# Optimization experiments

Hardware: AMD Instinct MI355X
Metric: run time of the kernel (lower is better)

Reference implementation:

```python
import jax, jax.numpy as jnp
import numpy as np

B, NR, NG = 16, 96, 64
AF, BF = 98, 6
H, QM, MAXNB, DEPTH = 300, 160, 10, 4
P = 2048
F = 2 * H + QM          # 760
D0 = F + 10             # 770


def _graph_idx(k, batch, n, idx_max):
    # gather_nd style indices (batch_idx, neighbor_idx): [batch, n, MAXNB, 2]
    nbr = jax.random.randint(k, (batch, n, MAXNB), 0, idx_max)
    b = jnp.broadcast_to(jnp.arange(batch)[:, None, None], (batch, n, MAXNB))
    return jnp.stack([b, nbr], axis=-1)


def setup_inputs() -> dict:
    key = jax.random.key(0)
    ks = jax.random.split(key, 32)
    f32 = jnp.float32
    inp = {}
    inp['res_atom'] = jax.random.normal(ks[0], (B, NR, AF), f32)
    inp['res_bond'] = jax.random.normal(ks[1], (B, NR, BF), f32)
    inp['res_atom_graph'] = _graph_idx(ks[2], B, NR, NR)
    inp['res_bond_graph'] = _graph_idx(ks[3], B, NR, NR)
    inp['res_num_nbs'] = jax.random.randint(ks[4], (B, NR), 1, MAXNB + 1)
    inp['res_node_mask'] = jnp.ones((B, NR, 1), f32)
    inp['rg_atom'] = jax.random.normal(ks[5], (B, NG, AF), f32)
    inp['rg_bond'] = jax.random.normal(ks[6], (B, NG, BF), f32)
    inp['rg_atom_graph'] = _graph_idx(ks[7], B, NG, NG)
    inp['rg_bond_graph'] = _graph_idx(ks[8], B, NG, NG)
    inp['rg_num_nbs'] = jax.random.randint(ks[9], (B, NG), 1, MAXNB + 1)
    inp['rg_node_mask'] = jnp.ones((B, NG, 1), f32)
    seg = jnp.repeat(jnp.arange(B), P // B)  # sorted reaction ids for segment_mean
    i = jax.random.randint(ks[10], (P,), 0, NR)
    j = jax.random.randint(ks[11], (P,), 0, NR)
    inp['core_mask'] = jnp.stack([seg, i, j], axis=-1)[None]   # [1, P, 3]
    inp['fatom_qm'] = jax.random.normal(ks[12], (B, NR, QM), f32)
    inp['connect'] = jax.random.normal(ks[13], (1, P, 10), f32)
    STD = 0.1  # keep relu chains alive at depth 4
    w = lambda k, shape: STD * jax.random.normal(k, shape, f32)
    for pre, kk in (('res', 14), ('rg', 20)):
        inp[pre + '_W_atom'] = w(ks[kk], (AF, H))
        inp[pre + '_W_nei_atom'] = w(ks[kk + 1], (H, H))
        inp[pre + '_W_nei_bond'] = w(ks[kk + 2], (BF, H))
        inp[pre + '_W_self'] = w(ks[kk + 3], (H, H))
        inp[pre + '_W_U2'] = w(ks[kk + 4], (H + BF, H))
        inp[pre + '_W_U1'] = w(ks[kk + 5], (2 * H, H))
    inp['W_att_h'] = w(ks[26], (H, H))
    inp['W_att_s'] = w(ks[27], (H, 1))
    inp['W_score0'] = 0.01 * jax.random.normal(ks[28], (D0, D0), f32)
    inp['W_score'] = 0.01 * jax.random.normal(ks[29], (D0, 1), f32)
    return inp


def _wln(atom, bond, atom_graph, bond_graph, num_nbs, node_mask,
         W_atom, W_nei_atom, W_nei_bond, W_self, W_U2, W_U1):
    relu = jax.nn.relu
    af = relu(atom @ W_atom)                                       # [B,N,H]
    mask = (jnp.arange(MAXNB)[None, None, :] < num_nbs[:, :, None])
    mask = mask.astype(af.dtype)[..., None]                        # [B,N,MAXNB,1]
    for _ in range(DEPTH):
        fa = af[atom_graph[..., 0], atom_graph[..., 1]]            # [B,N,MAXNB,H]
        fb = bond[bond_graph[..., 0], bond_graph[..., 1]]          # [B,N,MAXNB,BF]
        h_nei = relu(fa @ W_nei_atom) * relu(fb @ W_nei_bond)
        f_nei = jnp.sum(h_nei * mask, axis=2)                      # masked nbr sum
        kernels = f_nei * relu(af @ W_self) * node_mask
        pre = relu(jnp.concatenate([fa, fb], axis=3) @ W_U2)
        nei_label = jnp.sum(pre * mask, axis=2)
        af = relu(jnp.concatenate([af, nei_label], axis=2) @ W_U1)
    return kernels


def _forward(res_atom, res_bond, res_atom_graph, res_bond_graph, res_num_nbs, res_node_mask,
             rg_atom, rg_bond, rg_atom_graph, rg_bond_graph, rg_num_nbs, rg_node_mask,
             core_mask, fatom_qm, connect,
             res_W_atom, res_W_nei_atom, res_W_nei_bond, res_W_self, res_W_U2, res_W_U1,
             rg_W_atom, rg_W_nei_atom, rg_W_nei_bond, rg_W_self, rg_W_U2, rg_W_U1,
             W_att_h, W_att_s, W_score0, W_score):
    res_h = _wln(res_atom, res_bond, res_atom_graph, res_bond_graph, res_num_nbs, res_node_mask,
                 res_W_atom, res_W_nei_atom, res_W_nei_bond, res_W_self, res_W_U2, res_W_U1)
    rg_h = _wln(rg_atom, rg_bond, rg_atom_graph, rg_bond_graph, rg_num_nbs, rg_node_mask,
                rg_W_atom, rg_W_nei_atom, rg_W_nei_bond, rg_W_self, rg_W_U2, rg_W_U1)
    # Global attention: broadcast pairwise sum reactant x reagent atoms
    pair_att = res_h[:, :, None, :] + rg_h[:, None, :, :]          # [B,NR,NG,H]
    att = jax.nn.sigmoid(jax.nn.relu(pair_att @ W_att_h) @ W_att_s)
    ctx = jnp.sum(att * rg_h[:, None, :, :], axis=2)               # [B,NR,H]
    h = jnp.concatenate([res_h, ctx, fatom_qm], axis=-1)           # [B,NR,F]
    cm = core_mask[0]                                              # [P,3] = (b,i,j)
    # atom_pair[b,i,j] = h[b,i] + h[b,j]; gather only the core pairs (no N^2 tensor)
    pair = h[cm[:, 0], cm[:, 1]] + h[cm[:, 0], cm[:, 2]]           # [P,F]
    rh = jax.nn.relu(jnp.concatenate([pair, connect[0]], axis=-1) @ W_score0)
    seg = cm[:, 0]
    sums = jax.ops.segment_sum(rh, seg, num_segments=B)
    cnt = jax.ops.segment_sum(jnp.ones((P,), rh.dtype), seg, num_segments=B)
    mean = sums / cnt[:, None]                                     # segment_mean
    return mean @ W_score                                          # [B,1]


def reference(res_atom, res_bond, res_atom_graph, res_bond_graph, res_num_nbs, res_node_mask,
              rg_atom, rg_bond, rg_atom_graph, rg_bond_graph, rg_num_nbs, rg_node_mask,
              core_mask, fatom_qm, connect,
              res_W_atom, res_W_nei_atom, res_W_nei_bond, res_W_self, res_W_U2, res_W_U1,
              rg_W_atom, rg_W_nei_atom, rg_W_nei_bond, rg_W_self, rg_W_U2, rg_W_U1,
              W_att_h, W_att_s, W_score0, W_score):
    return _forward(res_atom, res_bond, res_atom_graph, res_bond_graph, res_num_nbs, res_node_mask,
                    rg_atom, rg_bond, rg_atom_graph, rg_bond_graph, rg_num_nbs, rg_node_mask,
                    core_mask, fatom_qm, connect,
                    res_W_atom, res_W_nei_atom, res_W_nei_bond, res_W_self, res_W_U2, res_W_U1,
                    rg_W_atom, rg_W_nei_atom, rg_W_nei_bond, rg_W_self, rg_W_U2, rg_W_U1,
                    W_att_h, W_att_s, W_score0, W_score)
```

## Files before the change

kernel.cpp:

```cpp
#include <hip/hip_runtime.h>


constexpr int cB = 16, cNR = 96, cNG = 64;
constexpr int cAF = 98, cBF = 6;
constexpr int cH = 300, cQM = 160, cMAXNB = 10, cDEPTH = 4;
constexpr int cP = 2048;
constexpr int cF = 2 * cH + cQM;
constexpr int cD0 = cF + 10;

constexpr int Mres = cB * cNR;
constexpr int Mrg  = cB * cNG;

typedef __attribute__((ext_vector_type(8))) short v8s;
typedef __attribute__((ext_vector_type(4))) float v4f;

__device__ inline unsigned short f2bf(float f) {
  unsigned u = __float_as_uint(f);
  u += 0x7FFF + ((u >> 16) & 1);
  return (unsigned short)(u >> 16);
}
__device__ inline float bf2f(unsigned short s) {
  return __uint_as_float(((unsigned)s) << 16);
}

struct PrepArg { const float* W; unsigned short* hiT; unsigned short* loT; int K; int N; int Kpad; };
struct PrepArgs { PrepArg a[16]; };

__global__ __launch_bounds__(256) void prep_k(PrepArgs pa)
{
  PrepArg p = pa.a[blockIdx.z];
  int idx = blockIdx.x * 256 + threadIdx.x;
  int total = p.N * p.Kpad;
  if (idx >= total) return;
  int n = idx / p.Kpad, k = idx - n * p.Kpad;
  float w = (k < p.K) ? p.W[(size_t)k * p.N + n] : 0.f;
  unsigned short h = f2bf(w);
  p.hiT[idx] = h;
  p.loT[idx] = f2bf(w - bf2f(h));
}

struct GArg {
  const float* A; const float* A2;
  const unsigned short* W1h; const unsigned short* W1l;
  const unsigned short* W2h; const unsigned short* W2l;
  float* C; int M; int K1; int Kp1; int K2; int Kp2; int act;
};
struct GArgs6 { GArg a[6]; };

#define MFMA __builtin_amdgcn_mfma_f32_16x16x32_bf16

__global__ __launch_bounds__(256) void gemm_mfma(GArgs6 ga, int N)
{
  GArg g = ga.a[blockIdx.z];
  int m0 = blockIdx.y * 64;
  if (m0 >= g.M) return;
  int n0 = blockIdx.x * 64;
  int nT = (g.Kp1 + g.Kp2) >> 5;

  __shared__ unsigned short Ah[2][64][40];
  __shared__ unsigned short Al[2][64][40];
  __shared__ unsigned short Bh[2][64][40];
  __shared__ unsigned short Bl[2][64][40];

  int tid = threadIdx.x;
  int sm = tid >> 2;
  int sk = (tid & 3) << 3;

  float areg[8];
  uint4 bh_reg, bl_reg;

  auto fetch = [&](int kv0) {
    int kv = kv0 + sk;
    const float* src; int kk, Klim;
    if (kv < g.Kp1) { src = g.A  + (size_t)(m0 + sm) * g.K1; kk = kv;          Klim = g.K1; }
    else            { src = g.A2 + (size_t)(m0 + sm) * g.K2; kk = kv - g.Kp1;  Klim = g.K2; }
    if (((Klim & 3) == 0) && kk + 7 < Klim) {
      float4 v0 = *(const float4*)(src + kk);
      float4 v1 = *(const float4*)(src + kk + 4);
      areg[0]=v0.x; areg[1]=v0.y; areg[2]=v0.z; areg[3]=v0.w;
      areg[4]=v1.x; areg[5]=v1.y; areg[6]=v1.z; areg[7]=v1.w;
    } else {
#pragma unroll
      for (int j = 0; j < 8; ++j) {
        int k = kk + j;
        areg[j] = (k < Klim) ? src[k] : 0.f;
      }
    }
    int gn = n0 + sm;
    if (gn < N) {
      const unsigned short *ph, *pl;
      if (kv < g.Kp1) { size_t o = (size_t)gn * g.Kp1 + kv;            ph = g.W1h + o; pl = g.W1l + o; }
      else            { size_t o = (size_t)gn * g.Kp2 + (kv - g.Kp1);  ph = g.W2h + o; pl = g.W2l + o; }
      bh_reg = *(const uint4*)ph;
      bl_reg = *(const uint4*)pl;
    } else {
      bh_reg = make_uint4(0,0,0,0); bl_reg = make_uint4(0,0,0,0);
    }
  };

  auto store = [&](int buf) {
    unsigned hs[8], ls[8];
#pragma unroll
    for (int j = 0; j < 8; ++j) {
      unsigned short h = f2bf(areg[j]);
      hs[j] = h;
      ls[j] = f2bf(areg[j] - bf2f(h));
    }
    uint4 hh, ll;
    hh.x = hs[0] | (hs[1] << 16); hh.y = hs[2] | (hs[3] << 16);
    hh.z = hs[4] | (hs[5] << 16); hh.w = hs[6] | (hs[7] << 16);
    ll.x = ls[0] | (ls[1] << 16); ll.y = ls[2] | (ls[3] << 16);
    ll.z = ls[4] | (ls[5] << 16); ll.w = ls[6] | (ls[7] << 16);
    *(uint4*)&Ah[buf][sm][sk] = hh;
    *(uint4*)&Al[buf][sm][sk] = ll;
    *(uint4*)&Bh[buf][sm][sk] = bh_reg;
    *(uint4*)&Bl[buf][sm][sk] = bl_reg;
  };

  int l = tid & 63, w = tid >> 6;
  int wm = (w >> 1) << 5, wn = (w & 1) << 5;
  int ar = wm + (l & 15), br = wn + (l & 15);
  int kc = (l >> 4) << 3;

  v4f acc00 = {0,0,0,0}, acc01 = {0,0,0,0}, acc10 = {0,0,0,0}, acc11 = {0,0,0,0};

  fetch(0); store(0); __syncthreads();
  for (int t = 0; t < nT; ++t) {
    if (t + 1 < nT) fetch((t + 1) << 5);
    int cur = t & 1;
    v8s ah0 = *(const v8s*)&Ah[cur][ar][kc];
    v8s ah1 = *(const v8s*)&Ah[cur][ar + 16][kc];
    v8s al0 = *(const v8s*)&Al[cur][ar][kc];
    v8s al1 = *(const v8s*)&Al[cur][ar + 16][kc];
    v8s bh0 = *(const v8s*)&Bh[cur][br][kc];
    v8s bh1 = *(const v8s*)&Bh[cur][br + 16][kc];
    v8s bl0 = *(const v8s*)&Bl[cur][br][kc];
    v8s bl1 = *(const v8s*)&Bl[cur][br + 16][kc];
    acc00 = MFMA(ah0, bh0, acc00, 0, 0, 0);
    acc00 = MFMA(ah0, bl0, acc00, 0, 0, 0);
    acc00 = MFMA(al0, bh0, acc00, 0, 0, 0);
    acc01 = MFMA(ah0, bh1, acc01, 0, 0, 0);
    acc01 = MFMA(ah0, bl1, acc01, 0, 0, 0);
    acc01 = MFMA(al0, bh1, acc01, 0, 0, 0);
    acc10 = MFMA(ah1, bh0, acc10, 0, 0, 0);
    acc10 = MFMA(ah1, bl0, acc10, 0, 0, 0);
    acc10 = MFMA(al1, bh0, acc10, 0, 0, 0);
    acc11 = MFMA(ah1, bh1, acc11, 0, 0, 0);
    acc11 = MFMA(ah1, bl1, acc11, 0, 0, 0);
    acc11 = MFMA(al1, bh1, acc11, 0, 0, 0);
    if (t + 1 < nT) store(cur ^ 1);
    __syncthreads();
  }

  int rbase = m0 + wm + ((l >> 4) << 2);
  int cbase = n0 + wn + (l & 15);
  auto wr = [&](v4f a, int fi, int fj) {
    int gn = cbase + fj * 16;
    if (gn >= N) return;
    float* Cp = g.C + (size_t)(rbase + fi * 16) * N + gn;
#pragma unroll
    for (int r = 0; r < 4; ++r) {
      float v = a[r];
      if (g.act) v = fmaxf(v, 0.f);
      Cp[(size_t)r * N] = v;
    }
  };
  wr(acc00, 0, 0); wr(acc01, 0, 1); wr(acc10, 1, 0); wr(acc11, 1, 1);
}

__global__ __launch_bounds__(256) void score_mfma_k(
    const float* __restrict__ h, const float* __restrict__ conn,
    const int* __restrict__ cm,
    const unsigned short* __restrict__ W0h, const unsigned short* __restrict__ W0l,
    const float* __restrict__ Wsc, float* __restrict__ pairsum)
{
  const int Kp = 800;
  const int nT = Kp >> 5;
  int m0 = blockIdx.y * 64;
  int n0 = blockIdx.x * 64;

  __shared__ unsigned short Ah[2][64][40];
  __shared__ unsigned short Al[2][64][40];
  __shared__ unsigned short Bh[2][64][40];
  __shared__ unsigned short Bl[2][64][40];

  int tid = threadIdx.x;
  int sm = tid >> 2;
  int sk = (tid & 3) << 3;

  int p = m0 + sm;
  int s3 = cm[p * 3 + 0];
  const float* h1 = h + (size_t)(s3 * cNR + cm[p * 3 + 1]) * cF;
  const float* h2 = h + (size_t)(s3 * cNR + cm[p * 3 + 2]) * cF;
  const float* cp = conn + (size_t)p * 10;

  float areg[8];
  uint4 bh_reg, bl_reg;

  auto fetch = [&](int kv0) {
    int kv = kv0 + sk;
    if (kv + 7 < cF) {
      float4 u = *(const float4*)(h1 + kv);
      float4 v = *(const float4*)(h2 + kv);
      float4 u2 = *(const float4*)(h1 + kv + 4);
      float4 v2 = *(const float4*)(h2 + kv + 4);
      areg[0]=u.x+v.x; areg[1]=u.y+v.y; areg[2]=u.z+v.z; areg[3]=u.w+v.w;
      areg[4]=u2.x+v2.x; areg[5]=u2.y+v2.y; areg[6]=u2.z+v2.z; areg[7]=u2.w+v2.w;
    } else {
#pragma unroll
      for (int j = 0; j < 8; ++j) {
        int k = kv + j;
        float v = 0.f;
        if (k < cF) v = h1[k] + h2[k];
        else if (k < cD0) v = cp[k - cF];
        areg[j] = v;
      }
    }
    int gn = n0 + sm;
    if (gn < cD0) {
      size_t o = (size_t)gn * Kp + kv;
      bh_reg = *(const uint4*)(W0h + o);
      bl_reg = *(const uint4*)(W0l + o);
    } else {
      bh_reg = make_uint4(0,0,0,0); bl_reg = make_uint4(0,0,0,0);
    }
  };

  auto store = [&](int buf) {
    unsigned hs[8], ls[8];
#pragma unroll
    for (int j = 0; j < 8; ++j) {
      unsigned short hv = f2bf(areg[j]);
      hs[j] = hv;
      ls[j] = f2bf(areg[j] - bf2f(hv));
    }
    uint4 hh, ll;
    hh.x = hs[0] | (hs[1] << 16); hh.y = hs[2] | (hs[3] << 16);
    hh.z = hs[4] | (hs[5] << 16); hh.w = hs[6] | (hs[7] << 16);
    ll.x = ls[0] | (ls[1] << 16); ll.y = ls[2] | (ls[3] << 16);
    ll.z = ls[4] | (ls[5] << 16); ll.w = ls[6] | (ls[7] << 16);
    *(uint4*)&Ah[buf][sm][sk] = hh;
    *(uint4*)&Al[buf][sm][sk] = ll;
    *(uint4*)&Bh[buf][sm][sk] = bh_reg;
    *(uint4*)&Bl[buf][sm][sk] = bl_reg;
  };

  int l = tid & 63, w = tid >> 6;
  int wm = (w >> 1) << 5, wn = (w & 1) << 5;
  int ar = wm + (l & 15), br = wn + (l & 15);
  int kc = (l >> 4) << 3;

  v4f acc00 = {0,0,0,0}, acc01 = {0,0,0,0}, acc10 = {0,0,0,0}, acc11 = {0,0,0,0};

  fetch(0); store(0); __syncthreads();
  for (int t = 0; t < nT; ++t) {
    if (t + 1 < nT) fetch((t + 1) << 5);
    int cur = t & 1;
    v8s ah0 = *(const v8s*)&Ah[cur][ar][kc];
    v8s ah1 = *(const v8s*)&Ah[cur][ar + 16][kc];
    v8s al0 = *(const v8s*)&Al[cur][ar][kc];
    v8s al1 = *(const v8s*)&Al[cur][ar + 16][kc];
    v8s bh0 = *(const v8s*)&Bh[cur][br][kc];
    v8s bh1 = *(const v8s*)&Bh[cur][br + 16][kc];
    v8s bl0 = *(const v8s*)&Bl[cur][br][kc];
    v8s bl1 = *(const v8s*)&Bl[cur][br + 16][kc];
    acc00 = MFMA(ah0, bh0, acc00, 0, 0, 0);
    acc00 = MFMA(ah0, bl0, acc00, 0, 0, 0);
    acc00 = MFMA(al0, bh0, acc00, 0, 0, 0);
    acc01 = MFMA(ah0, bh1, acc01, 0, 0, 0);
    acc01 = MFMA(ah0, bl1, acc01, 0, 0, 0);
    acc01 = MFMA(al0, bh1, acc01, 0, 0, 0);
    acc10 = MFMA(ah1, bh0, acc10, 0, 0, 0);
    acc10 = MFMA(ah1, bl0, acc10, 0, 0, 0);
    acc10 = MFMA(al1, bh0, acc10, 0, 0, 0);
    acc11 = MFMA(ah1, bh1, acc11, 0, 0, 0);
    acc11 = MFMA(ah1, bl1, acc11, 0, 0, 0);
    acc11 = MFMA(al1, bh1, acc11, 0, 0, 0);
    if (t + 1 < nT) store(cur ^ 1);
    __syncthreads();
  }

  int cbase = n0 + wn + (l & 15);
  float w0 = (cbase      < cD0) ? Wsc[cbase]      : 0.f;
  float w1 = (cbase + 16 < cD0) ? Wsc[cbase + 16] : 0.f;
  float ps[8];
#pragma unroll
  for (int r = 0; r < 4; ++r) {
    ps[r]     = fmaxf(acc00[r], 0.f) * w0 + fmaxf(acc01[r], 0.f) * w1;
    ps[4 + r] = fmaxf(acc10[r], 0.f) * w0 + fmaxf(acc11[r], 0.f) * w1;
  }
#pragma unroll
  for (int m = 1; m < 16; m <<= 1) {
#pragma unroll
    for (int q = 0; q < 8; ++q) ps[q] += __shfl_xor(ps[q], m, 64);
  }
  if ((l & 15) == 0) {
#pragma unroll
    for (int q = 0; q < 8; ++q) {
      int gm = m0 + wm + (q >> 2) * 16 + ((l >> 4) << 2) + (q & 3);
      atomicAdd(&pairsum[gm], ps[q]);
    }
  }
}

__global__ __launch_bounds__(320) void nei_label2_k(
    const float* __restrict__ RaR, const float* __restrict__ RbR,
    const int* __restrict__ agR, const int* __restrict__ bgR,
    const int* __restrict__ nnbR, float* __restrict__ outR,
    const float* __restrict__ RaG, const float* __restrict__ RbG,
    const int* __restrict__ agG, const int* __restrict__ bgG,
    const int* __restrict__ nnbG, float* __restrict__ outG)
{
  int node = blockIdx.x;
  const float *Ra, *Rb; const int *ag, *bg, *nnb; float* out; int Nn, loc;
  if (node < Mres) { Ra=RaR; Rb=RbR; ag=agR; bg=bgR; nnb=nnbR; out=outR; Nn=cNR; loc=node; }
  else { Ra=RaG; Rb=RbG; ag=agG; bg=bgG; nnb=nnbG; out=outG; Nn=cNG; loc=node-Mres; }
  int h = threadIdx.x;
  int nn = nnb[loc];
  const int* agp = ag + (size_t)loc * cMAXNB * 2;
  const int* bgp = bg + (size_t)loc * cMAXNB * 2;
  if (h < cH) {
    float s = 0.f;
    for (int k = 0; k < nn; ++k) {
      int ra = agp[2 * k] * Nn + agp[2 * k + 1];
      int rb = bgp[2 * k] * Nn + bgp[2 * k + 1];
      s += fmaxf(Ra[(size_t)ra * cH + h] + Rb[(size_t)rb * cH + h], 0.f);
    }
    out[(size_t)loc * cH + h] = s;
  }
}

__global__ __launch_bounds__(320) void kernels2_k(
    const float* __restrict__ SaR, const float* __restrict__ SbR,
    const float* __restrict__ SelfR_R,
    const int* __restrict__ agR, const int* __restrict__ bgR,
    const int* __restrict__ nnbR, const float* __restrict__ maskR,
    float* __restrict__ outR,
    const float* __restrict__ SaG, const float* __restrict__ SbG,
    const float* __restrict__ SelfR_G,
    const int* __restrict__ agG, const int* __restrict__ bgG,
    const int* __restrict__ nnbG, const float* __restrict__ maskG,
    float* __restrict__ outG)
{
  int node = blockIdx.x;
  const float *Sa, *Sb, *Se, *mk; const int *ag, *bg, *nnb; float* out; int Nn, loc;
  if (node < Mres) { Sa=SaR; Sb=SbR; Se=SelfR_R; ag=agR; bg=bgR; nnb=nnbR; mk=maskR; out=outR; Nn=cNR; loc=node; }
  else { Sa=SaG; Sb=SbG; Se=SelfR_G; ag=agG; bg=bgG; nnb=nnbG; mk=maskG; out=outG; Nn=cNG; loc=node-Mres; }
  int h = threadIdx.x;
  int nn = nnb[loc];
  const int* agp = ag + (size_t)loc * cMAXNB * 2;
  const int* bgp = bg + (size_t)loc * cMAXNB * 2;
  if (h < cH) {
    float s = 0.f;
    for (int k = 0; k < nn; ++k) {
      int ra = agp[2 * k] * Nn + agp[2 * k + 1];
      int rb = bgp[2 * k] * Nn + bgp[2 * k + 1];
      s += Sa[(size_t)ra * cH + h] * Sb[(size_t)rb * cH + h];
    }
    out[(size_t)loc * cH + h] = s * Se[(size_t)loc * cH + h] * mk[loc];
  }
}

#define AIT 4
__global__ __launch_bounds__(256) void att_ctx_h_k(
    const float* __restrict__ U, const float* __restrict__ V,
    const float* __restrict__ att_w, const float* __restrict__ rgh,
    const float* __restrict__ kern, const float* __restrict__ qm,
    float* __restrict__ h)
{
  __shared__ float attL[AIT][cNG];
  int blk = blockIdx.x;
  int b = blk / (cNR / AIT);
  int it = blk - b * (cNR / AIT);
  int row0 = b * cNR + it * AIT;
  int tid = threadIdx.x, lane = tid & 63, w = tid >> 6;
  int n0 = lane * 4, n1 = 256 + lane * 4;
  bool v1 = (lane < 11);
  float4 z4 = make_float4(0.f, 0.f, 0.f, 0.f);

  float4 u[AIT][2], wv[2];
  wv[0] = *(const float4*)(att_w + n0);
  wv[1] = v1 ? *(const float4*)(att_w + n1) : z4;
#pragma unroll
  for (int i = 0; i < AIT; ++i) {
    const float* Ur = U + (size_t)(row0 + i) * cH;
    u[i][0] = *(const float4*)(Ur + n0);
    u[i][1] = v1 ? *(const float4*)(Ur + n1) : z4;
  }

  for (int r = 0; r < 4; ++r) {
    int jb = w * 16 + r * 4;
    float4 vv[4][2];
#pragma unroll
    for (int q = 0; q < 4; ++q) {
      const float* Vr = V + (size_t)(b * cNG + jb + q) * cH;
      vv[q][0] = *(const float4*)(Vr + n0);
      vv[q][1] = v1 ? *(const float4*)(Vr + n1) : z4;
    }
    float s[4][AIT];
#pragma unroll
    for (int q = 0; q < 4; ++q)
#pragma unroll
      for (int i = 0; i < AIT; ++i) {
        float acc = 0.f;
#pragma unroll
        for (int pp = 0; pp < 2; ++pp) {
          float4 uu = u[i][pp], vq = vv[q][pp], ww = wv[pp];
          acc += fmaxf(uu.x + vq.x, 0.f) * ww.x;
          acc += fmaxf(uu.y + vq.y, 0.f) * ww.y;
          acc += fmaxf(uu.z + vq.z, 0.f) * ww.z;
          acc += fmaxf(uu.w + vq.w, 0.f) * ww.w;
        }
        s[q][i] = acc;
      }
#pragma unroll
    for (int m = 1; m < 64; m <<= 1)
#pragma unroll
      for (int q = 0; q < 4; ++q)
#pragma unroll
        for (int i = 0; i < AIT; ++i)
          s[q][i] += __shfl_xor(s[q][i], m);
    if (lane < 16) {
      float sv = 0.f;
#pragma unroll
      for (int q = 0; q < 4; ++q)
#pragma unroll
        for (int i = 0; i < AIT; ++i)
          if (lane == q * 4 + i) sv = s[q][i];
      attL[lane & 3][jb + (lane >> 2)] = 1.f / (1.f + expf(-sv));
    }
  }
  __syncthreads();

  const float* rgb = rgh + (size_t)b * cNG * cH;
  float* hrow = h + (size_t)(row0 + w) * cF;
  for (int c = lane; c < 75; c += 64) {
    float4 p = z4;
    for (int j = 0; j < cNG; ++j) {
      float aj = attL[w][j];
      float4 rv = *(const float4*)(rgb + (size_t)j * cH + c * 4);
      p.x += aj * rv.x; p.y += aj * rv.y; p.z += aj * rv.z; p.w += aj * rv.w;
    }
    *(float4*)(hrow + cH + c * 4) = p;
  }
  for (int idx = tid; idx < AIT * 75; idx += 256) {
    int i = idx / 75, c = idx - i * 75;
    *(float4*)(h + (size_t)(row0 + i) * cF + c * 4) =
        *(const float4*)(kern + (size_t)(row0 + i) * cH + c * 4);
  }
  for (int idx = tid; idx < AIT * 40; idx += 256) {
    int i = idx / 40, c = idx - i * 40;
    *(float4*)(h + (size_t)(row0 + i) * cF + 2 * cH + c * 4) =
        *(const float4*)(qm + (size_t)(row0 + i) * cQM + c * 4);
  }
}

__global__ void seg_final_k(const float* __restrict__ ps,
                            const int* __restrict__ cm, float* __restrict__ out)
{
  __shared__ float s[cB];
  int tid = threadIdx.x;
  if (tid < cB) s[tid] = 0.f;
  __syncthreads();
  for (int p = tid; p < cP; p += 256) atomicAdd(&s[cm[p * 3]], ps[p]);
  __syncthreads();
  if (tid < cB) out[tid] = s[tid] * (1.f / 128.f);
}

extern "C" void kernel_launch(void* const* d_in, const int* in_sizes, int n_in,
                              void* d_out, int out_size, void* d_ws, size_t ws_size,
                              hipStream_t stream)
{
  (void)in_sizes; (void)n_in; (void)out_size; (void)ws_size;
  const float* res_atom = (const float*)d_in[0];
  const float* res_bond = (const float*)d_in[1];
  const int*   res_ag   = (const int*)d_in[2];
  const int*   res_bg   = (const int*)d_in[3];
  const int*   res_nnb  = (const int*)d_in[4];
  const float* res_mask = (const float*)d_in[5];
  const float* rg_atom  = (const float*)d_in[6];
  const float* rg_bond  = (const float*)d_in[7];
  const int*   rg_ag    = (const int*)d_in[8];
  const int*   rg_bg    = (const int*)d_in[9];
  const int*   rg_nnb   = (const int*)d_in[10];
  const float* rg_mask  = (const float*)d_in[11];
  const int*   core     = (const int*)d_in[12];
  const float* qm       = (const float*)d_in[13];
  const float* connect  = (const float*)d_in[14];
  const float* Wm[2][6];
  for (int s = 0; s < 2; ++s)
    for (int k = 0; k < 6; ++k) Wm[s][k] = (const float*)d_in[15 + s * 6 + k];
  const float* W_att_h  = (const float*)d_in[27];
  const float* W_att_s  = (const float*)d_in[28];
  const float* W_score0 = (const float*)d_in[29];
  const float* W_score  = (const float*)d_in[30];
  float* out = (float*)d_out;

  float* ws = (float*)d_ws;
  size_t off = 0;
  auto alloc = [&](size_t nfloat) {
    float* p = ws + off;
    off += (nfloat + 63) & ~(size_t)63;
    return p;
  };
  auto allocU = [&](size_t nush) {
    return (unsigned short*)alloc((nush + 1) / 2);
  };

  float* afA_r = alloc((size_t)Mres * cH);
  float* afB_r = alloc((size_t)Mres * cH);
  float* Rb_r  = alloc((size_t)Mres * cH);
  float* Sb_r  = alloc((size_t)Mres * cH);
  float* Ra_r  = alloc((size_t)Mres * cH);
  float* nei_r = alloc((size_t)Mres * cH);
  float* kern_r= alloc((size_t)Mres * cH);
  float* afA_g = alloc((size_t)Mrg * cH);
  float* afB_g = alloc((size_t)Mrg * cH);
  float* Rb_g  = alloc((size_t)Mrg * cH);
  float* Sb_g  = alloc((size_t)Mrg * cH);
  float* Ra_g  = alloc((size_t)Mrg * cH);
  float* nei_g = alloc((size_t)Mrg * cH);
  float* kern_g= alloc((size_t)Mrg * cH);
  float* U     = alloc((size_t)Mres * cH);
  float* V     = alloc((size_t)Mrg * cH);
  float* h760  = alloc((size_t)Mres * cF);
  float* pairsum = alloc(cP);

  struct WT { unsigned short *h, *l; int K, Kp; const float* src; };
  auto rup32 = [](int k) { return (k + 31) & ~31; };
  WT t[2][8];
  for (int s = 0; s < 2; ++s) {
    const int Ks[8] = {cAF, cH, cBF, cH, cH, cBF, cH, cH};
    const float* srcs[8] = {
      Wm[s][0], Wm[s][1], Wm[s][2], Wm[s][3],
      Wm[s][4], Wm[s][4] + (size_t)cH * cH,
      Wm[s][5], Wm[s][5] + (size_t)cH * cH };
    for (int k = 0; k < 8; ++k) {
      int Kp = rup32(Ks[k]);
      t[s][k].K = Ks[k]; t[s][k].Kp = Kp; t[s][k].src = srcs[k];
      t[s][k].h = allocU((size_t)cH * Kp);
      t[s][k].l = allocU((size_t)cH * Kp);
    }
  }
  unsigned short* attT_h = allocU((size_t)cH * 320);
  unsigned short* attT_l = allocU((size_t)cH * 320);
  unsigned short* sc0T_h = allocU((size_t)cD0 * 800);
  unsigned short* sc0T_l = allocU((size_t)cD0 * 800);

  {
    PrepArgs pa{};
    for (int s = 0; s < 2; ++s)
      for (int k = 0; k < 8; ++k)
        pa.a[s * 8 + k] = {t[s][k].src, t[s][k].h, t[s][k].l, t[s][k].K, cH, t[s][k].Kp};
    dim3 grid((cH * 320 + 255) / 256, 1, 16);
    prep_k<<<grid, dim3(256), 0, stream>>>(pa);
  }
  {
    PrepArgs pa{};
    pa.a[0] = {W_att_h,  attT_h, attT_l, cH, cH, 320};
    pa.a[1] = {W_score0, sc0T_h, sc0T_l, cD0, cD0, 800};
    dim3 grid((cD0 * 800 + 255) / 256, 1, 2);
    prep_k<<<grid, dim3(256), 0, stream>>>(pa);
  }

  dim3 blk(256);
  GArg zero{};
  auto launch = [&](GArgs6& ga, int nprob) {
    dim3 grid(5, Mres / 64, nprob);
    gemm_mfma<<<grid, blk, 0, stream>>>(ga, cH);
  };

  {
    GArgs6 ga{{
      {res_atom, nullptr, t[0][0].h, t[0][0].l, nullptr, nullptr, afA_r, Mres, cAF, 128, 0, 0, 1},
      {rg_atom,  nullptr, t[1][0].h, t[1][0].l, nullptr, nullptr, afA_g, Mrg,  cAF, 128, 0, 0, 1},
      {res_bond, nullptr, t[0][5].h, t[0][5].l, nullptr, nullptr, Rb_r,  Mres, cBF, 32,  0, 0, 0},
      {rg_bond,  nullptr, t[1][5].h, t[1][5].l, nullptr, nullptr, Rb_g,  Mrg,  cBF, 32,  0, 0, 0},
      {res_bond, nullptr, t[0][2].h, t[0][2].l, nullptr, nullptr, Sb_r,  Mres, cBF, 32,  0, 0, 1},
      {rg_bond,  nullptr, t[1][2].h, t[1][2].l, nullptr, nullptr, Sb_g,  Mrg,  cBF, 32,  0, 0, 1},
    }};
    launch(ga, 6);
  }

  float* af_r = afA_r; float* afo_r = afB_r;
  float* af_g = afA_g; float* afo_g = afB_g;
  for (int it = 0; it < cDEPTH - 1; ++it) {
    {
      GArgs6 ga{{
        {af_r, nullptr, t[0][4].h, t[0][4].l, nullptr, nullptr, Ra_r, Mres, cH, 320, 0, 0, 0},
        {af_g, nullptr, t[1][4].h, t[1][4].l, nullptr, nullptr, Ra_g, Mrg,  cH, 320, 0, 0, 0},
        zero, zero, zero, zero,
      }};
      launch(ga, 2);
    }
    nei_label2_k<<<dim3(Mres + Mrg), dim3(320), 0, stream>>>(
        Ra_r, Rb_r, res_ag, res_bg, res_nnb, nei_r,
        Ra_g, Rb_g, rg_ag, rg_bg, rg_nnb, nei_g);
    {
      GArgs6 ga{{
        {af_r, nei_r, t[0][6].h, t[0][6].l, t[0][7].h, t[0][7].l, afo_r, Mres, cH, 320, cH, 320, 1},
        {af_g, nei_g, t[1][6].h, t[1][6].l, t[1][7].h, t[1][7].l, afo_g, Mrg,  cH, 320, cH, 320, 1},
        zero, zero, zero, zero,
      }};
      launch(ga, 2);
    }
    { float* tmp = af_r; af_r = afo_r; afo_r = tmp; }
    { float* tmp = af_g; af_g = afo_g; afo_g = tmp; }
  }

  {
    GArgs6 ga{{
      {af_r, nullptr, t[0][1].h, t[0][1].l, nullptr, nullptr, Ra_r,  Mres, cH, 320, 0, 0, 1},
      {af_g, nullptr, t[1][1].h, t[1][1].l, nullptr, nullptr, Ra_g,  Mrg,  cH, 320, 0, 0, 1},
      {af_r, nullptr, t[0][3].h, t[0][3].l, nullptr, nullptr, nei_r, Mres, cH, 320, 0, 0, 1},
      {af_g, nullptr, t[1][3].h, t[1][3].l, nullptr, nullptr, nei_g, Mrg,  cH, 320, 0, 0, 1},
      zero, zero,
    }};
    launch(ga, 4);
  }
  kernels2_k<<<dim3(Mres + Mrg), dim3(320), 0, stream>>>(
      Ra_r, Sb_r, nei_r, res_ag, res_bg, res_nnb, res_mask, kern_r,
      Ra_g, Sb_g, nei_g, rg_ag, rg_bg, rg_nnb, rg_mask, kern_g);

  {
    GArgs6 ga{{
      {kern_r, nullptr, attT_h, attT_l, nullptr, nullptr, U, Mres, cH, 320, 0, 0, 0},
      {kern_g, nullptr, attT_h, attT_l, nullptr, nullptr, V, Mrg,  cH, 320, 0, 0, 0},
      zero, zero, zero, zero,
    }};
    launch(ga, 2);
  }
  att_ctx_h_k<<<dim3(cB * (cNR / AIT)), dim3(256), 0, stream>>>(
      U, V, W_att_s, kern_g, kern_r, qm, h760);

  hipMemsetAsync(pairsum, 0, cP * sizeof(float), stream);
  score_mfma_k<<<dim3(13, cP / 64), blk, 0, stream>>>(
      h760, connect, core, sc0T_h, sc0T_l, W_score, pairsum);
  seg_final_k<<<dim3(1), dim3(256), 0, stream>>>(pairsum, core, out);
}
```

Measured before the change: 270.3 us.

## Fuse neighbor gather into GEMM A-load and concatenate weight matrices

Removes the separate neighbor-label kernel: the U1 GEMM now builds its A operand on the fly by gathering and summing relu(Ra+Rb) over neighbors. The self half of U1 is computed in the same GEMM as W_U2 through concatenated weights, and its result is added as a bias in the epilogue. Final-stage Ra/self GEMMs are likewise merged into one N=600 GEMM. The two prep launches and the pairsum memset are folded into a single prep kernel. The cost is redundant gather work: every N-column block of the GEMM recomputes the same neighbor sums.

```diff
diff --git a/kernel.cpp b/kernel.cpp
--- a/kernel.cpp
+++ b/kernel.cpp
@@ -23,27 +23,34 @@
   return __uint_as_float(((unsigned)s) << 16);
 }
 
-struct PrepArg { const float* W; unsigned short* hiT; unsigned short* loT; int K; int N; int Kpad; };
-struct PrepArgs { PrepArg a[16]; };
+struct PrepEnt { const float* W; unsigned short* hiT; unsigned short* loT;
+                 int K, N, Kpad; };
+struct PrepArgs { PrepEnt e[19]; int bases[20]; int nent; };
 
 __global__ __launch_bounds__(256) void prep_k(PrepArgs pa)
 {
-  PrepArg p = pa.a[blockIdx.z];
-  int idx = blockIdx.x * 256 + threadIdx.x;
-  int total = p.N * p.Kpad;
-  if (idx >= total) return;
-  int n = idx / p.Kpad, k = idx - n * p.Kpad;
+  int g = blockIdx.x * 256 + threadIdx.x;
+  if (g >= pa.bases[pa.nent]) return;
+  int idx = 0;
+  while (g >= pa.bases[idx + 1]) ++idx;
+  PrepEnt p = pa.e[idx];
+  int local = g - pa.bases[idx];
+  if (!p.W) { ((float*)p.hiT)[local] = 0.f; return; }
+  int n = local / p.Kpad, k = local - n * p.Kpad;
   float w = (k < p.K) ? p.W[(size_t)k * p.N + n] : 0.f;
   unsigned short h = f2bf(w);
-  p.hiT[idx] = h;
-  p.loT[idx] = f2bf(w - bf2f(h));
+  p.hiT[local] = h;
+  p.loT[local] = f2bf(w - bf2f(h));
 }
 
 struct GArg {
-  const float* A; const float* A2;
-  const unsigned short* W1h; const unsigned short* W1l;
-  const unsigned short* W2h; const unsigned short* W2l;
-  float* C; int M; int K1; int Kp1; int K2; int Kp2; int act;
+  const float* A;
+  const float* Ra; const float* Rb;
+  const int* ag; const int* bg; const int* nnb; int NnIdx; int ldRa;
+  const unsigned short* Wh; const unsigned short* Wl;
+  const float* bias; int ldBias;
+  float* C; int ldC;
+  int M, K, Kp, act;
 };
 struct GArgs6 { GArg a[6]; };
 
@@ -55,7 +62,7 @@
   int m0 = blockIdx.y * 64;
   if (m0 >= g.M) return;
   int n0 = blockIdx.x * 64;
-  int nT = (g.Kp1 + g.Kp2) >> 5;
+  int nT = g.Kp >> 5;
 
   __shared__ unsigned short Ah[2][64][40];
   __shared__ unsigned short Al[2][64][40];
@@ -65,34 +72,63 @@
   int tid = threadIdx.x;
   int sm = tid >> 2;
   int sk = (tid & 3) << 3;
+  int gm = m0 + sm;
+
+  int nn = 0; const int *agp = nullptr, *bgp = nullptr;
+  if (!g.A) {
+    nn = g.nnb[gm];
+    agp = g.ag + (size_t)gm * 2 * cMAXNB;
+    bgp = g.bg + (size_t)gm * 2 * cMAXNB;
+  }
 
   float areg[8];
   uint4 bh_reg, bl_reg;
 
   auto fetch = [&](int kv0) {
-    int kv = kv0 + sk;
-    const float* src; int kk, Klim;
-    if (kv < g.Kp1) { src = g.A  + (size_t)(m0 + sm) * g.K1; kk = kv;          Klim = g.K1; }
-    else            { src = g.A2 + (size_t)(m0 + sm) * g.K2; kk = kv - g.Kp1;  Klim = g.K2; }
-    if (((Klim & 3) == 0) && kk + 7 < Klim) {
-      float4 v0 = *(const float4*)(src + kk);
-      float4 v1 = *(const float4*)(src + kk + 4);
-      areg[0]=v0.x; areg[1]=v0.y; areg[2]=v0.z; areg[3]=v0.w;
-      areg[4]=v1.x; areg[5]=v1.y; areg[6]=v1.z; areg[7]=v1.w;
+    int kk = kv0 + sk;
+    if (g.A) {
+      const float* src = g.A + (size_t)gm * g.K;
+      if (((g.K & 3) == 0) && kk + 7 < g.K) {
+        float4 v0 = *(const float4*)(src + kk);
+        float4 v1 = *(const float4*)(src + kk + 4);
+        areg[0]=v0.x; areg[1]=v0.y; areg[2]=v0.z; areg[3]=v0.w;
+        areg[4]=v1.x; areg[5]=v1.y; areg[6]=v1.z; areg[7]=v1.w;
+      } else {
+#pragma unroll
+        for (int j = 0; j < 8; ++j) areg[j] = (kk + j < g.K) ? src[kk + j] : 0.f;
+      }
     } else {
-#pragma unroll
-      for (int j = 0; j < 8; ++j) {
-        int k = kk + j;
-        areg[j] = (k < Klim) ? src[k] : 0.f;
+      float acc[8] = {0.f,0.f,0.f,0.f,0.f,0.f,0.f,0.f};
+      if (kk < g.K) {
+        for (int k = 0; k < nn; ++k) {
+          int ra = agp[2 * k] * g.NnIdx + agp[2 * k + 1];
+          int rb = bgp[2 * k] * g.NnIdx + bgp[2 * k + 1];
+          const float* pa = g.Ra + (size_t)ra * g.ldRa + kk;
+          const float* pb = g.Rb + (size_t)rb * cH + kk;
+          float4 a0 = *(const float4*)pa, a1 = *(const float4*)(pa + 4);
+          float4 b0 = *(const float4*)pb, b1 = *(const float4*)(pb + 4);
+          acc[0] += fmaxf(a0.x + b0.x, 0.f);
+          acc[1] += fmaxf(a0.y + b0.y, 0.f);
+          acc[2] += fmaxf(a0.z + b0.z, 0.f);
+          acc[3] += fmaxf(a0.w + b0.w, 0.f);
+          acc[4] += fmaxf(a1.x + b1.x, 0.f);
+          acc[5] += fmaxf(a1.y + b1.y, 0.f);
+          acc[6] += fmaxf(a1.z + b1.z, 0.f);
+          acc[7] += fmaxf(a1.w + b1.w, 0.f);
+        }
+        if (kk + 8 > g.K) {
+#pragma unroll
+          for (int j = 0; j < 8; ++j) if (kk + j >= g.K) acc[j] = 0.f;
+        }
       }
+#pragma unroll
+      for (int j = 0; j < 8; ++j) areg[j] = acc[j];
     }
     int gn = n0 + sm;
     if (gn < N) {
-      const unsigned short *ph, *pl;
-      if (kv < g.Kp1) { size_t o = (size_t)gn * g.Kp1 + kv;            ph = g.W1h + o; pl = g.W1l + o; }
-      else            { size_t o = (size_t)gn * g.Kp2 + (kv - g.Kp1);  ph = g.W2h + o; pl = g.W2l + o; }
-      bh_reg = *(const uint4*)ph;
-      bl_reg = *(const uint4*)pl;
+      size_t o = (size_t)gn * g.Kp + kv0 + sk;
+      bh_reg = *(const uint4*)(g.Wh + o);
+      bl_reg = *(const uint4*)(g.Wl + o);
     } else {
       bh_reg = make_uint4(0,0,0,0); bl_reg = make_uint4(0,0,0,0);
     }
@@ -102,9 +138,9 @@
     unsigned hs[8], ls[8];
 #pragma unroll
     for (int j = 0; j < 8; ++j) {
-      unsigned short h = f2bf(areg[j]);
-      hs[j] = h;
-      ls[j] = f2bf(areg[j] - bf2f(h));
+      unsigned short hv = f2bf(areg[j]);
+      hs[j] = hv;
+      ls[j] = f2bf(areg[j] - bf2f(hv));
     }
     uint4 hh, ll;
     hh.x = hs[0] | (hs[1] << 16); hh.y = hs[2] | (hs[3] << 16);
@@ -157,12 +193,15 @@
   auto wr = [&](v4f a, int fi, int fj) {
     int gn = cbase + fj * 16;
     if (gn >= N) return;
-    float* Cp = g.C + (size_t)(rbase + fi * 16) * N + gn;
+    float* Cp = g.C + (size_t)(rbase + fi * 16) * g.ldC + gn;
+    const float* Bp = g.bias ? g.bias + (size_t)(rbase + fi * 16) * g.ldBias + gn
+                             : nullptr;
 #pragma unroll
     for (int r = 0; r < 4; ++r) {
       float v = a[r];
+      if (Bp) v += Bp[(size_t)r * g.ldBias];
       if (g.act) v = fmaxf(v, 0.f);
-      Cp[(size_t)r * N] = v;
+      Cp[(size_t)r * g.ldC] = v;
     }
   };
   wr(acc00, 0, 0); wr(acc01, 0, 1); wr(acc10, 1, 0); wr(acc11, 1, 1);
@@ -303,18 +342,20 @@
   }
 }
 
-__global__ __launch_bounds__(320) void nei_label2_k(
-    const float* __restrict__ RaR, const float* __restrict__ RbR,
+__global__ __launch_bounds__(320) void kernels2_k(
+    const float* __restrict__ SaSeR, const float* __restrict__ SbR,
     const int* __restrict__ agR, const int* __restrict__ bgR,
-    const int* __restrict__ nnbR, float* __restrict__ outR,
-    const float* __restrict__ RaG, const float* __restrict__ RbG,
+    const int* __restrict__ nnbR, const float* __restrict__ maskR,
+    float* __restrict__ outR,
+    const float* __restrict__ SaSeG, const float* __restrict__ SbG,
     const int* __restrict__ agG, const int* __restrict__ bgG,
-    const int* __restrict__ nnbG, float* __restrict__ outG)
+    const int* __restrict__ nnbG, const float* __restrict__ maskG,
+    float* __restrict__ outG)
 {
   int node = blockIdx.x;
-  const float *Ra, *Rb; const int *ag, *bg, *nnb; float* out; int Nn, loc;
-  if (node < Mres) { Ra=RaR; Rb=RbR; ag=agR; bg=bgR; nnb=nnbR; out=outR; Nn=cNR; loc=node; }
-  else { Ra=RaG; Rb=RbG; ag=agG; bg=bgG; nnb=nnbG; out=outG; Nn=cNG; loc=node-Mres; }
+  const float *SaSe, *Sb, *mk; const int *ag, *bg, *nnb; float* out; int Nn, loc;
+  if (node < Mres) { SaSe=SaSeR; Sb=SbR; ag=agR; bg=bgR; nnb=nnbR; mk=maskR; out=outR; Nn=cNR; loc=node; }
+  else { SaSe=SaSeG; Sb=SbG; ag=agG; bg=bgG; nnb=nnbG; mk=maskG; out=outG; Nn=cNG; loc=node-Mres; }
   int h = threadIdx.x;
   int nn = nnb[loc];
   const int* agp = ag + (size_t)loc * cMAXNB * 2;
@@ -324,40 +365,9 @@
     for (int k = 0; k < nn; ++k) {
       int ra = agp[2 * k] * Nn + agp[2 * k + 1];
       int rb = bgp[2 * k] * Nn + bgp[2 * k + 1];
-      s += fmaxf(Ra[(size_t)ra * cH + h] + Rb[(size_t)rb * cH + h], 0.f);
-    }
-    out[(size_t)loc * cH + h] = s;
-  }
-}
-
-__global__ __launch_bounds__(320) void kernels2_k(
-    const float* __restrict__ SaR, const float* __restrict__ SbR,
-    const float* __restrict__ SelfR_R,
-    const int* __restrict__ agR, const int* __restrict__ bgR,
-    const int* __restrict__ nnbR, const float* __restrict__ maskR,
-    float* __restrict__ outR,
-    const float* __restrict__ SaG, const float* __restrict__ SbG,
-    const float* __restrict__ SelfR_G,
-    const int* __restrict__ agG, const int* __restrict__ bgG,
-    const int* __restrict__ nnbG, const float* __restrict__ maskG,
-    float* __restrict__ outG)
-{
-  int node = blockIdx.x;
-  const float *Sa, *Sb, *Se, *mk; const int *ag, *bg, *nnb; float* out; int Nn, loc;
-  if (node < Mres) { Sa=SaR; Sb=SbR; Se=SelfR_R; ag=agR; bg=bgR; nnb=nnbR; mk=maskR; out=outR; Nn=cNR; loc=node; }
-  else { Sa=SaG; Sb=SbG; Se=SelfR_G; ag=agG; bg=bgG; nnb=nnbG; mk=maskG; out=outG; Nn=cNG; loc=node-Mres; }
-  int h = threadIdx.x;
-  int nn = nnb[loc];
-  const int* agp = ag + (size_t)loc * cMAXNB * 2;
-  const int* bgp = bg + (size_t)loc * cMAXNB * 2;
-  if (h < cH) {
-    float s = 0.f;
-    for (int k = 0; k < nn; ++k) {
-      int ra = agp[2 * k] * Nn + agp[2 * k + 1];
-      int rb = bgp[2 * k] * Nn + bgp[2 * k + 1];
-      s += Sa[(size_t)ra * cH + h] * Sb[(size_t)rb * cH + h];
-    }
-    out[(size_t)loc * cH + h] = s * Se[(size_t)loc * cH + h] * mk[loc];
+      s += SaSe[(size_t)ra * 600 + h] * Sb[(size_t)rb * cH + h];
+    }
+    out[(size_t)loc * cH + h] = s * SaSe[(size_t)loc * 600 + 300 + h] * mk[loc];
   }
 }
 
@@ -507,79 +517,100 @@
     return (unsigned short*)alloc((nush + 1) / 2);
   };
 
-  float* afA_r = alloc((size_t)Mres * cH);
-  float* afB_r = alloc((size_t)Mres * cH);
-  float* Rb_r  = alloc((size_t)Mres * cH);
-  float* Sb_r  = alloc((size_t)Mres * cH);
-  float* Ra_r  = alloc((size_t)Mres * cH);
-  float* nei_r = alloc((size_t)Mres * cH);
-  float* kern_r= alloc((size_t)Mres * cH);
-  float* afA_g = alloc((size_t)Mrg * cH);
-  float* afB_g = alloc((size_t)Mrg * cH);
-  float* Rb_g  = alloc((size_t)Mrg * cH);
-  float* Sb_g  = alloc((size_t)Mrg * cH);
-  float* Ra_g  = alloc((size_t)Mrg * cH);
-  float* nei_g = alloc((size_t)Mrg * cH);
-  float* kern_g= alloc((size_t)Mrg * cH);
-  float* U     = alloc((size_t)Mres * cH);
-  float* V     = alloc((size_t)Mrg * cH);
-  float* h760  = alloc((size_t)Mres * cF);
+  float* afA_r  = alloc((size_t)Mres * cH);
+  float* afB_r  = alloc((size_t)Mres * cH);
+  float* Rb_r   = alloc((size_t)Mres * cH);
+  float* Sb_r   = alloc((size_t)Mres * cH);
+  float* RaU1_r = alloc((size_t)Mres * 600);
+  float* kern_r = alloc((size_t)Mres * cH);
+  float* afA_g  = alloc((size_t)Mrg * cH);
+  float* afB_g  = alloc((size_t)Mrg * cH);
+  float* Rb_g   = alloc((size_t)Mrg * cH);
+  float* Sb_g   = alloc((size_t)Mrg * cH);
+  float* RaU1_g = alloc((size_t)Mrg * 600);
+  float* kern_g = alloc((size_t)Mrg * cH);
+  float* U      = alloc((size_t)Mres * cH);
+  float* V      = alloc((size_t)Mrg * cH);
+  float* h760   = alloc((size_t)Mres * cF);
   float* pairsum = alloc(cP);
 
-  struct WT { unsigned short *h, *l; int K, Kp; const float* src; };
-  auto rup32 = [](int k) { return (k + 31) & ~31; };
-  WT t[2][8];
+  unsigned short *atomT_h[2], *atomT_l[2], *nbT_h[2], *nbT_l[2];
+  unsigned short *U2bT_h[2], *U2bT_l[2], *cat1_h[2], *cat1_l[2];
+  unsigned short *cat2_h[2], *cat2_l[2], *U1bT_h[2], *U1bT_l[2];
   for (int s = 0; s < 2; ++s) {
-    const int Ks[8] = {cAF, cH, cBF, cH, cH, cBF, cH, cH};
-    const float* srcs[8] = {
-      Wm[s][0], Wm[s][1], Wm[s][2], Wm[s][3],
-      Wm[s][4], Wm[s][4] + (size_t)cH * cH,
-      Wm[s][5], Wm[s][5] + (size_t)cH * cH };
-    for (int k = 0; k < 8; ++k) {
-      int Kp = rup32(Ks[k]);
-      t[s][k].K = Ks[k]; t[s][k].Kp = Kp; t[s][k].src = srcs[k];
-      t[s][k].h = allocU((size_t)cH * Kp);
-      t[s][k].l = allocU((size_t)cH * Kp);
-    }
-  }
-  unsigned short* attT_h = allocU((size_t)cH * 320);
-  unsigned short* attT_l = allocU((size_t)cH * 320);
-  unsigned short* sc0T_h = allocU((size_t)cD0 * 800);
-  unsigned short* sc0T_l = allocU((size_t)cD0 * 800);
+    atomT_h[s] = allocU((size_t)300 * 128); atomT_l[s] = allocU((size_t)300 * 128);
+    nbT_h[s]   = allocU((size_t)300 * 32);  nbT_l[s]   = allocU((size_t)300 * 32);
+    U2bT_h[s]  = allocU((size_t)300 * 32);  U2bT_l[s]  = allocU((size_t)300 * 32);
+    cat1_h[s]  = allocU((size_t)600 * 320); cat1_l[s]  = allocU((size_t)600 * 320);
+    cat2_h[s]  = allocU((size_t)600 * 320); cat2_l[s]  = allocU((size_t)600 * 320);
+    U1bT_h[s]  = allocU((size_t)300 * 320); U1bT_l[s]  = allocU((size_t)300 * 320);
+  }
+  unsigned short* attT_h = allocU((size_t)300 * 320);
+  unsigned short* attT_l = allocU((size_t)300 * 320);
+  unsigned short* sc0T_h = allocU((size_t)770 * 800);
+  unsigned short* sc0T_l = allocU((size_t)770 * 800);
 
   {
     PrepArgs pa{};
-    for (int s = 0; s < 2; ++s)
-      for (int k = 0; k < 8; ++k)
-        pa.a[s * 8 + k] = {t[s][k].src, t[s][k].h, t[s][k].l, t[s][k].K, cH, t[s][k].Kp};
-    dim3 grid((cH * 320 + 255) / 256, 1, 16);
-    prep_k<<<grid, dim3(256), 0, stream>>>(pa);
-  }
-  {
-    PrepArgs pa{};
-    pa.a[0] = {W_att_h,  attT_h, attT_l, cH, cH, 320};
-    pa.a[1] = {W_score0, sc0T_h, sc0T_l, cD0, cD0, 800};
-    dim3 grid((cD0 * 800 + 255) / 256, 1, 2);
-    prep_k<<<grid, dim3(256), 0, stream>>>(pa);
+    int e = 0, base = 0;
+    auto add = [&](const float* W, unsigned short* ht, unsigned short* lt,
+                   int K, int N, int Kp) {
+      pa.e[e] = {W, ht, lt, K, N, Kp};
+      pa.bases[e] = base;
+      base += N * Kp;
+      ++e;
+    };
+    for (int s = 0; s < 2; ++s) {
+      add(Wm[s][0], atomT_h[s], atomT_l[s], cAF, cH, 128);
+      add(Wm[s][2], nbT_h[s],   nbT_l[s],   cBF, cH, 32);
+      add(Wm[s][4] + (size_t)cH * cH, U2bT_h[s], U2bT_l[s], cBF, cH, 32);
+      add(Wm[s][4], cat1_h[s],               cat1_l[s],               cH, cH, 320);
+      add(Wm[s][5], cat1_h[s] + 300 * 320,   cat1_l[s] + 300 * 320,   cH, cH, 320);
+      add(Wm[s][1], cat2_h[s],               cat2_l[s],               cH, cH, 320);
+      add(Wm[s][3], cat2_h[s] + 300 * 320,   cat2_l[s] + 300 * 320,   cH, cH, 320);
+      add(Wm[s][5] + (size_t)cH * cH, U1bT_h[s], U1bT_l[s], cH, cH, 320);
+    }
+    add(W_att_h,  attT_h, attT_l, cH, cH, 320);
+    add(W_score0, sc0T_h, sc0T_l, cD0, cD0, 800);
+    pa.e[e] = {nullptr, (unsigned short*)pairsum, nullptr, 0, 0, 0};
+    pa.bases[e] = base; base += cP; ++e;
+    pa.bases[e] = base;
+    pa.nent = e;
+    prep_k<<<dim3((base + 255) / 256), dim3(256), 0, stream>>>(pa);
   }
 
   dim3 blk(256);
   GArg zero{};
-  auto launch = [&](GArgs6& ga, int nprob) {
-    dim3 grid(5, Mres / 64, nprob);
-    gemm_mfma<<<grid, blk, 0, stream>>>(ga, cH);
+  auto gplain = [&](const float* A, const unsigned short* Wh, const unsigned short* Wl,
+                    float* C, int ldC, int M, int K, int Kp, int act,
+                    const float* bias = nullptr, int ldb = 0) {
+    GArg g{};
+    g.A = A; g.Wh = Wh; g.Wl = Wl; g.bias = bias; g.ldBias = ldb;
+    g.C = C; g.ldC = ldC; g.M = M; g.K = K; g.Kp = Kp; g.act = act;
+    return g;
+  };
+  auto ggather = [&](const float* Ra, int ldRa, const float* Rb,
+                     const int* ag, const int* bg, const int* nnb, int Nn,
+                     const unsigned short* Wh, const unsigned short* Wl,
+                     float* C, int ldC, int M, int K, int Kp, int act,
+                     const float* bias, int ldb) {
+    GArg g{};
+    g.Ra = Ra; g.ldRa = ldRa; g.Rb = Rb; g.ag = ag; g.bg = bg; g.nnb = nnb;
+    g.NnIdx = Nn; g.Wh = Wh; g.Wl = Wl; g.bias = bias; g.ldBias = ldb;
+    g.C = C; g.ldC = ldC; g.M = M; g.K = K; g.Kp = Kp; g.act = act;
+    return g;
   };
 
   {
     GArgs6 ga{{
-      {res_atom, nullptr, t[0][0].h, t[0][0].l, nullptr, nullptr, afA_r, Mres, cAF, 128, 0, 0, 1},
-      {rg_atom,  nullptr, t[1][0].h, t[1][0].l, nullptr, nullptr, afA_g, Mrg,  cAF, 128, 0, 0, 1},
-      {res_bond, nullptr, t[0][5].h, t[0][5].l, nullptr, nullptr, Rb_r,  Mres, cBF, 32,  0, 0, 0},
-      {rg_bond,  nullptr, t[1][5].h, t[1][5].l, nullptr, nullptr, Rb_g,  Mrg,  cBF, 32,  0, 0, 0},
-      {res_bond, nullptr, t[0][2].h, t[0][2].l, nullptr, nullptr, Sb_r,  Mres, cBF, 32,  0, 0, 1},
-      {rg_bond,  nullptr, t[1][2].h, t[1][2].l, nullptr, nullptr, Sb_g,  Mrg,  cBF, 32,  0, 0, 1},
+      gplain(res_atom, atomT_h[0], atomT_l[0], afA_r, cH, Mres, cAF, 128, 1),
+      gplain(rg_atom,  atomT_h[1], atomT_l[1], afA_g, cH, Mrg,  cAF, 128, 1),
+      gplain(res_bond, U2bT_h[0],  U2bT_l[0],  Rb_r,  cH, Mres, cBF, 32, 0),
+      gplain(rg_bond,  U2bT_h[1],  U2bT_l[1],  Rb_g,  cH, Mrg,  cBF, 32, 0),
+      gplain(res_bond, nbT_h[0],   nbT_l[0],   Sb_r,  cH, Mres, cBF, 32, 1),
+      gplain(rg_bond,  nbT_h[1],   nbT_l[1],   Sb_g,  cH, Mrg,  cBF, 32, 1),
     }};
-    launch(ga, 6);
+    gemm_mfma<<<dim3(5, 24, 6), blk, 0, stream>>>(ga, cH);
   }
 
   float* af_r = afA_r; float* afo_r = afB_r;
@@ -587,22 +618,23 @@
   for (int it = 0; it < cDEPTH - 1; ++it) {
     {
       GArgs6 ga{{
-        {af_r, nullptr, t[0][4].h, t[0][4].l, nullptr, nullptr, Ra_r, Mres, cH, 320, 0, 0, 0},
-        {af_g, nullptr, t[1][4].h, t[1][4].l, nullptr, nullptr, Ra_g, Mrg,  cH, 320, 0, 0, 0},
+        gplain(af_r, cat1_h[0], cat1_l[0], RaU1_r, 600, Mres, cH, 320, 0),
+        gplain(af_g, cat1_h[1], cat1_l[1], RaU1_g, 600, Mrg,  cH, 320, 0),
         zero, zero, zero, zero,
       }};
-      launch(ga, 2);
-    }
-    nei_label2_k<<<dim3(Mres + Mrg), dim3(320), 0, stream>>>(
-        Ra_r, Rb_r, res_ag, res_bg, res_nnb, nei_r,
-        Ra_g, Rb_g, rg_ag, rg_bg, rg_nnb, nei_g);
+      gemm_mfma<<<dim3(10, 24, 2), blk, 0, stream>>>(ga, 600);
+    }
     {
       GArgs6 ga{{
-        {af_r, nei_r, t[0][6].h, t[0][6].l, t[0][7].h, t[0][7].l, afo_r, Mres, cH, 320, cH, 320, 1},
-        {af_g, nei_g, t[1][6].h, t[1][6].l, t[1][7].h, t[1][7].l, afo_g, Mrg,  cH, 320, cH, 320, 1},
+        ggather(RaU1_r, 600, Rb_r, res_ag, res_bg, res_nnb, cNR,
+                U1bT_h[0], U1bT_l[0], afo_r, cH, Mres, cH, 320, 1,
+                RaU1_r + 300, 600),
+        ggather(RaU1_g, 600, Rb_g, rg_ag, rg_bg, rg_nnb, cNG,
+                U1bT_h[1], U1bT_l[1], afo_g, cH, Mrg, cH, 320, 1,
+                RaU1_g + 300, 600),
         zero, zero, zero, zero,
       }};
-      launch(ga, 2);
+      gemm_mfma<<<dim3(5, 24, 2), blk, 0, stream>>>(ga, cH);
     }
     { float* tmp = af_r; af_r = afo_r; afo_r = tmp; }
     { float* tmp = af_g; af_g = afo_g; afo_g = tmp; }
@@ -610,30 +642,27 @@
 
   {
     GArgs6 ga{{
-      {af_r, nullptr, t[0][1].h, t[0][1].l, nullptr, nullptr, Ra_r,  Mres, cH, 320, 0, 0, 1},
-      {af_g, nullptr, t[1][1].h, t[1][1].l, nullptr, nullptr, Ra_g,  Mrg,  cH, 320, 0, 0, 1},
-      {af_r, nullptr, t[0][3].h, t[0][3].l, nullptr, nullptr, nei_r, Mres, cH, 320, 0, 0, 1},
-      {af_g, nullptr, t[1][3].h, t[1][3].l, nullptr, nullptr, nei_g, Mrg,  cH, 320, 0, 0, 1},
-      zero, zero,
+      gplain(af_r, cat2_h[0], cat2_l[0], RaU1_r, 600, Mres, cH, 320, 1),
+      gplain(af_g, cat2_h[1], cat2_l[1], RaU1_g, 600, Mrg,  cH, 320, 1),
+      zero, zero, zero, zero,
     }};
-    launch(ga, 4);
+    gemm_mfma<<<dim3(10, 24, 2), blk, 0, stream>>>(ga, 600);
   }
   kernels2_k<<<dim3(Mres + Mrg), dim3(320), 0, stream>>>(
-      Ra_r, Sb_r, nei_r, res_ag, res_bg, res_nnb, res_mask, kern_r,
-      Ra_g, Sb_g, nei_g, rg_ag, rg_bg, rg_nnb, rg_mask, kern_g);
+      RaU1_r, Sb_r, res_ag, res_bg, res_nnb, res_mask, kern_r,
+      RaU1_g, Sb_g, rg_ag, rg_bg, rg_nnb, rg_mask, kern_g);
 
   {
     GArgs6 ga{{
-      {kern_r, nullptr, attT_h, attT_l, nullptr, nullptr, U, Mres, cH, 320, 0, 0, 0},
-      {kern_g, nullptr, attT_h, attT_l, nullptr, nullptr, V, Mrg,  cH, 320, 0, 0, 0},
+      gplain(kern_r, attT_h, attT_l, U, cH, Mres, cH, 320, 0),
+      gplain(kern_g, attT_h, attT_l, V, cH, Mrg,  cH, 320, 0),
       zero, zero, zero, zero,
     }};
-    launch(ga, 2);
+    gemm_mfma<<<dim3(5, 24, 2), blk, 0, stream>>>(ga, cH);
   }
   att_ctx_h_k<<<dim3(cB * (cNR / AIT)), dim3(256), 0, stream>>>(
       U, V, W_att_s, kern_g, kern_r, qm, h760);
 
-  hipMemsetAsync(pairsum, 0, cP * sizeof(float), stream);
   score_mfma_k<<<dim3(13, cP / 64), blk, 0, stream>>>(
       h760, connect, core, sc0T_h, sc0T_l, W_score, pairsum);
   seg_final_k<<<dim3(1), dim3(256), 0, stream>>>(pairsum, core, out);
```

New measurement: 385.4 us. +42.6%, slower.
